# Kernel tuning notes

Hardware: AMD Instinct MI355X
Metric: run time of the kernel (lower is better)

## Reference

```python
import jax, jax.numpy as jnp
import numpy as np
from jax import lax

C = 384  # in_planes


def setup_inputs() -> dict:
    key = jax.random.key(0)
    k1, k2 = jax.random.split(key)
    x = jax.random.normal(k1, (16, C, 128, 128), dtype=jnp.float32)
    k = jax.random.normal(k2, (C, 1, 3, 3), dtype=jnp.float32)  # (in_planes, 1, kh, kw)
    return {"x": x, "k": k}


def reference(x, k):
    # Depthwise conv: equivalent to the original per-channel F.conv2d loop + concat,
    # fused into a single grouped conv with feature_group_count = C.
    return lax.conv_general_dilated(
        x, k,
        window_strides=(1, 1),
        padding=((1, 1), (1, 1)),
        rhs_dilation=(1, 1),
        dimension_numbers=("NCHW", "OIHW", "NCHW"),
        feature_group_count=C,
    )
```

## Files before the change

kernel.cpp:

```cpp
#include <hip/hip_runtime.h>


#define CC 384
#define HH 128
#define WW 128
#define NN 16

__global__ __launch_bounds__(256) void dwconv3x3(const float* __restrict__ x,
                                                 const float* __restrict__ k,
                                                 float* __restrict__ out) {
    const int nc = blockIdx.x;
    const int c  = nc % CC;

    const int tid   = (int)threadIdx.x;
    const int w_idx = tid & 31;
    const int w0    = w_idx << 2;
    const int h0    = (tid >> 5) << 4;

    const float* xp = x   + (size_t)nc * (HH * WW);
    float*       op = out + (size_t)nc * (HH * WW);

    const float* kp = k + c * 9;
    const float w00 = kp[0], w01 = kp[1], w02 = kp[2];
    const float w10 = kp[3], w11 = kp[4], w12 = kp[5];
    const float w20 = kp[6], w21 = kp[7], w22 = kp[8];

    const bool lEdge = (w_idx == 0);
    const bool rEdge = (w_idx == 31);

    float r[3][6];

#define LOAD_ROW(h, ri)                                                        \
    {                                                                          \
        float4 m = make_float4(0.f, 0.f, 0.f, 0.f);                            \
        if ((unsigned)(h) < (unsigned)HH)                                      \
            m = *reinterpret_cast<const float4*>(xp + (h) * WW + w0);          \
        r[ri][1] = m.x; r[ri][2] = m.y; r[ri][3] = m.z; r[ri][4] = m.w;        \
        const float lv = __shfl_up(m.w, 1);                                    \
        const float rv = __shfl_down(m.x, 1);                                  \
        r[ri][0] = lEdge ? 0.f : lv;                                           \
        r[ri][5] = rEdge ? 0.f : rv;                                           \
    }

    LOAD_ROW(h0 - 1, 0)
    LOAD_ROW(h0,     1)

    #pragma unroll
    for (int i = 0; i < 16; ++i) {
        const int h = h0 + i;
        LOAD_ROW(h + 1, (i + 2) % 3)

        float o[4];
        #pragma unroll
        for (int j = 0; j < 4; ++j) {
            o[j] = r[i % 3][j]           * w00 + r[i % 3][j + 1]       * w01
                 + r[i % 3][j + 2]       * w02
                 + r[(i + 1) % 3][j]     * w10 + r[(i + 1) % 3][j + 1] * w11
                 + r[(i + 1) % 3][j + 2] * w12
                 + r[(i + 2) % 3][j]     * w20 + r[(i + 2) % 3][j + 1] * w21
                 + r[(i + 2) % 3][j + 2] * w22;
        }
        *reinterpret_cast<float4*>(op + h * WW + w0) =
            make_float4(o[0], o[1], o[2], o[3]);
    }
#undef LOAD_ROW
}

extern "C" void kernel_launch(void* const* d_in, const int* in_sizes, int n_in,
                              void* d_out, int out_size, void* d_ws, size_t ws_size,
                              hipStream_t stream) {
    const float* x = (const float*)d_in[0];
    const float* k = (const float*)d_in[1];
    float*     out = (float*)d_out;

    const int blocks = NN * CC;
    dwconv3x3<<<blocks, 256, 0, stream>>>(x, k, out);
}
```

Baseline: 164.0 us.

## Stage input tile in LDS and split each plane across two blocks

Each block now loads a 66-row halo tile of one channel plane into shared memory in a single batched phase, then computes 64 output rows from LDS. Warp shuffles for the horizontal halo are replaced by LDS reads. The grid is doubled so each plane is handled by two blocks. This raises memory-level parallelism and block count, at the cost of about 34 KB of LDS per block, a barrier, and redundant halo row loads.

After: 152.1 us. -7.2%, faster.

```diff
diff --git a/kernel.cpp b/kernel.cpp
--- a/kernel.cpp
+++ b/kernel.cpp
@@ -9,46 +9,60 @@
 __global__ __launch_bounds__(256) void dwconv3x3(const float* __restrict__ x,
                                                  const float* __restrict__ k,
                                                  float* __restrict__ out) {
-    const int nc = blockIdx.x;
-    const int c  = nc % CC;
+    __shared__ float lds[66][WW];
 
-    const int tid   = (int)threadIdx.x;
-    const int w_idx = tid & 31;
-    const int w0    = w_idx << 2;
-    const int h0    = (tid >> 5) << 4;
+    const int b     = blockIdx.x;
+    const int half  = b & 1;
+    const int nc    = b >> 1;
+    const int c     = nc % CC;
+    const int hbase = half * 64;
 
     const float* xp = x   + (size_t)nc * (HH * WW);
     float*       op = out + (size_t)nc * (HH * WW);
+
+    const int tid = (int)threadIdx.x;
+
+    #pragma unroll
+    for (int it = 0; it < 9; ++it) {
+        const int s = tid + it * 256;
+        if (s < 66 * 32) {
+            const int row = s >> 5;
+            const int col = (s & 31) << 2;
+            const int h   = hbase - 1 + row;
+            float4 m = make_float4(0.f, 0.f, 0.f, 0.f);
+            if ((unsigned)h < (unsigned)HH)
+                m = *reinterpret_cast<const float4*>(xp + h * WW + col);
+            *reinterpret_cast<float4*>(&lds[row][col]) = m;
+        }
+    }
 
     const float* kp = k + c * 9;
     const float w00 = kp[0], w01 = kp[1], w02 = kp[2];
     const float w10 = kp[3], w11 = kp[4], w12 = kp[5];
     const float w20 = kp[6], w21 = kp[7], w22 = kp[8];
 
-    const bool lEdge = (w_idx == 0);
-    const bool rEdge = (w_idx == 31);
+    __syncthreads();
+
+    const int w0   = (tid & 31) << 2;
+    const int hloc = (tid >> 5) << 3;
 
     float r[3][6];
 
-#define LOAD_ROW(h, ri)                                                        \
+#define LDSROW(ri, rr)                                                         \
     {                                                                          \
-        float4 m = make_float4(0.f, 0.f, 0.f, 0.f);                            \
-        if ((unsigned)(h) < (unsigned)HH)                                      \
-            m = *reinterpret_cast<const float4*>(xp + (h) * WW + w0);          \
+        const float* p = &lds[(rr)][0];                                        \
+        const float4 m = *reinterpret_cast<const float4*>(p + w0);             \
         r[ri][1] = m.x; r[ri][2] = m.y; r[ri][3] = m.z; r[ri][4] = m.w;        \
-        const float lv = __shfl_up(m.w, 1);                                    \
-        const float rv = __shfl_down(m.x, 1);                                  \
-        r[ri][0] = lEdge ? 0.f : lv;                                           \
-        r[ri][5] = rEdge ? 0.f : rv;                                           \
+        r[ri][0] = (w0 > 0)      ? p[w0 - 1] : 0.f;                            \
+        r[ri][5] = (w0 + 4 < WW) ? p[w0 + 4] : 0.f;                            \
     }
 
-    LOAD_ROW(h0 - 1, 0)
-    LOAD_ROW(h0,     1)
+    LDSROW(0, hloc)
+    LDSROW(1, hloc + 1)
 
     #pragma unroll
-    for (int i = 0; i < 16; ++i) {
-        const int h = h0 + i;
-        LOAD_ROW(h + 1, (i + 2) % 3)
+    for (int i = 0; i < 8; ++i) {
+        LDSROW((i + 2) % 3, hloc + i + 2)
 
         float o[4];
         #pragma unroll
@@ -60,10 +74,10 @@
                  + r[(i + 2) % 3][j]     * w20 + r[(i + 2) % 3][j + 1] * w21
                  + r[(i + 2) % 3][j + 2] * w22;
         }
-        *reinterpret_cast<float4*>(op + h * WW + w0) =
+        *reinterpret_cast<float4*>(op + (hbase + hloc + i) * WW + w0) =
             make_float4(o[0], o[1], o[2], o[3]);
     }
-#undef LOAD_ROW
+#undef LDSROW
 }
 
 extern "C" void kernel_launch(void* const* d_in, const int* in_sizes, int n_in,
@@ -73,6 +87,6 @@
     const float* k = (const float*)d_in[1];
     float*     out = (float*)d_out;
 
-    const int blocks = NN * CC;
+    const int blocks = NN * CC * 2;
     dwconv3x3<<<blocks, 256, 0, stream>>>(x, k, out);
 }
```
